# Kernel tuning notes

Measured on AMD Instinct MI355X. Metric: run time of the kernel, lower is better.

Reference implementation:

```python
import jax, jax.numpy as jnp
import numpy as np

N, E = 50000, 800000
IN, EIN, HID, OUT = 128, 64, 64, 64
NEG_SLOPE = 0.2


def setup_inputs() -> dict:
    key = jax.random.key(0)
    ks = jax.random.split(key, 24)
    p = lambda k, shape: jax.random.normal(k, shape, jnp.float32) * 0.05
    return {
        'x': jax.random.normal(ks[0], (N, IN), jnp.float32),
        'edge_index': jax.random.randint(ks[1], (2, E), 0, N, jnp.int64),
        'edge_attr': jax.random.normal(ks[2], (E, EIN), jnp.float32),
        'batch': jnp.sort(jax.random.randint(ks[3], (N,), 0, 64, jnp.int64)),
        # GATConv 1 (in -> hidden, edge_dim=EIN)
        'W1': p(ks[4], (IN, HID)), 'a_src1': p(ks[5], (HID,)), 'a_dst1': p(ks[6], (HID,)),
        'We1': p(ks[7], (EIN, HID)), 'a_e1': p(ks[8], (HID,)), 'b1': jnp.zeros((HID,), jnp.float32),
        # GATConv 2 (hidden -> out)
        'W2': p(ks[9], (HID, OUT)), 'a_src2': p(ks[10], (OUT,)), 'a_dst2': p(ks[11], (OUT,)),
        'We2': p(ks[12], (EIN, OUT)), 'a_e2': p(ks[13], (OUT,)), 'b2': jnp.zeros((OUT,), jnp.float32),
        # edge MLP
        'Wm1': p(ks[14], (EIN, HID)), 'bm1': jnp.zeros((HID,), jnp.float32),
        'Wm2': p(ks[15], (HID, OUT)), 'bm2': jnp.zeros((OUT,), jnp.float32),
    }


def _gat(x, src, dst, edge_attr, W, a_s, a_d, We, a_e, b, n):
    # PyG GATConv (heads=1): add self-loops with edge_attr fill_value='mean'
    ones = jnp.ones((src.shape[0],), x.dtype)
    deg = jax.ops.segment_sum(ones, dst, num_segments=n)
    loop_attr = jax.ops.segment_sum(edge_attr, dst, num_segments=n) / jnp.maximum(deg, 1.0)[:, None]
    ar = jnp.arange(n)
    src2 = jnp.concatenate([src, ar])
    dst2 = jnp.concatenate([dst, ar])
    ea = jnp.concatenate([edge_attr, loop_attr], axis=0)  # [E+N, EIN]
    h = x @ W                                             # [N, C]
    a_src = h @ a_s                                       # [N]
    a_dst = h @ a_d                                       # [N]
    a_edge = (ea @ We) @ a_e                              # [E+N]
    alpha = jax.nn.leaky_relu(a_src[src2] + a_dst[dst2] + a_edge, NEG_SLOPE)
    # scatter-softmax over incoming edges of each dst node
    amax = jax.ops.segment_max(alpha, dst2, num_segments=n)
    ex = jnp.exp(alpha - amax[dst2])
    denom = jax.ops.segment_sum(ex, dst2, num_segments=n)
    coef = ex / denom[dst2]                               # [E+N]
    out = jax.ops.segment_sum(h[src2] * coef[:, None], dst2, num_segments=n)
    return out + b


def reference(x, edge_index, edge_attr, batch,
              W1, a_src1, a_dst1, We1, a_e1, b1,
              W2, a_src2, a_dst2, We2, a_e2, b2,
              Wm1, bm1, Wm2, bm2):
    n = x.shape[0]
    src, dst = edge_index[0], edge_index[1]
    h = _gat(x, src, dst, edge_attr, W1, a_src1, a_dst1, We1, a_e1, b1, n)
    h = jax.nn.elu(h)
    h = _gat(h, src, dst, edge_attr, W2, a_src2, a_dst2, We2, a_e2, b2, n)
    e = jax.nn.relu(edge_attr @ Wm1 + bm1) @ Wm2 + bm2
    return h, e, batch
```

## Files before the change

### kernel.cpp

```cpp
#include <hip/hip_runtime.h>

constexpr int NN = 50000;
constexpr int NE = 800000;
constexpr int C = 64;
constexpr int IN_DIM = 128;
constexpr float NEG = 0.2f;
constexpr int NB = (NN + 255) / 256;

typedef __attribute__((ext_vector_type(8))) short short8;
typedef __attribute__((ext_vector_type(4))) float f32x4;

__device__ __forceinline__ unsigned short f2bf(float f) {
    unsigned u = __float_as_uint(f);
    unsigned r = 0x7FFFu + ((u >> 16) & 1u);
    return (unsigned short)((u + r) >> 16);
}
__device__ __forceinline__ unsigned pack_bf2(float a, float b) {
    return (unsigned)f2bf(a) | ((unsigned)f2bf(b) << 16);
}
__device__ __forceinline__ float bf2f(unsigned u) {
    return __uint_as_float(u << 16);
}

__global__ __launch_bounds__(256) void k_setup(
        const float* __restrict__ We1, const float* __restrict__ ae1v,
        const float* __restrict__ We2, const float* __restrict__ ae2v,
        const float* __restrict__ W1, const float* __restrict__ as1,
        const float* __restrict__ ad1,
        const float* __restrict__ W2, const float* __restrict__ as2,
        const float* __restrict__ ad2,
        const int* __restrict__ batch,
        float* __restrict__ vecs, int* __restrict__ hist, int* __restrict__ bagg,
        float* __restrict__ out_b) {
    int t = blockIdx.x * 256 + threadIdx.x;
    if (t < 512) {
        const float* M; const float* v; int row;
        if      (t < 64)  { M = We1; v = ae1v; row = t; }
        else if (t < 128) { M = We2; v = ae2v; row = t - 64; }
        else if (t < 256) { M = W1;  v = as1;  row = t - 128; }
        else if (t < 384) { M = W1;  v = ad1;  row = t - 256; }
        else if (t < 448) { M = W2;  v = as2;  row = t - 384; }
        else              { M = W2;  v = ad2;  row = t - 448; }
        float s = 0.f;
        #pragma unroll
        for (int c = 0; c < 64; ++c) s += M[row * 64 + c] * v[c];
        vecs[t] = s;
    }
    if (t < NN) { hist[t] = 0; out_b[t] = (float)batch[t]; }
    if (t < NB) bagg[t] = 0;
}

__global__ __launch_bounds__(256) void k_mlp_mfma(
        const float* __restrict__ ea, const int* __restrict__ dst,
        const float* __restrict__ Wm1, const float* __restrict__ bm1,
        const float* __restrict__ Wm2, const float* __restrict__ bm2,
        const float* __restrict__ wv,
        float* __restrict__ eout, float* __restrict__ ae1, float* __restrict__ ae2,
        int* __restrict__ hist) {
    constexpr int AP = 144;
    __shared__ char Atile[128 * AP];
    __shared__ char Bt1[64 * AP];
    __shared__ char Bt2[64 * AP];
    const int t = threadIdx.x;
    const long long E0 = (long long)blockIdx.x * 128;
    const int l = t & 63;

    if (t < 128) atomicAdd(&hist[dst[E0 + t]], 1);

    {
        const int j = t & 15;
        const int eb = t >> 4;
        float4 wk1 = *(const float4*)&wv[j * 4];
        float4 wk2 = *(const float4*)&wv[64 + j * 4];
        const f32x4* g = (const f32x4*)(ea + E0 * 64);
        float s1[8], s2[8];
        #pragma unroll
        for (int q = 0; q < 8; ++q) {
            f32x4 v = __builtin_nontemporal_load(&g[t + 256 * q]);
            int e = eb + 16 * q;
            s1[q] = v[0] * wk1.x + v[1] * wk1.y + v[2] * wk1.z + v[3] * wk1.w;
            s2[q] = v[0] * wk2.x + v[1] * wk2.y + v[2] * wk2.z + v[3] * wk2.w;
            uint2 wr;
            wr.x = pack_bf2(v[0], v[1]);
            wr.y = pack_bf2(v[2], v[3]);
            *(uint2*)(Atile + e * AP + j * 8) = wr;
        }
        #pragma unroll
        for (int off = 1; off < 16; off <<= 1) {
            #pragma unroll
            for (int q = 0; q < 8; ++q) {
                s1[q] += __shfl_xor(s1[q], off);
                s2[q] += __shfl_xor(s2[q], off);
            }
        }
        float o1 = 0.f, o2 = 0.f;
        #pragma unroll
        for (int q = 0; q < 8; ++q) {
            if (j == q)     o1 = s1[q];
            if (j == q + 8) o2 = s2[q];
        }
        if (j < 8) ae1[E0 + eb + 16 * j] = o1;
        else       ae2[E0 + eb + 16 * (j - 8)] = o2;
    }
    {
        const int c = t & 63, kq = t >> 6;
        #pragma unroll
        for (int i = 0; i < 16; i += 2) {
            int k = kq * 16 + i;
            *(unsigned*)(Bt1 + c * AP + k * 2) = pack_bf2(Wm1[k * 64 + c], Wm1[(k + 1) * 64 + c]);
            *(unsigned*)(Bt2 + c * AP + k * 2) = pack_bf2(Wm2[k * 64 + c], Wm2[(k + 1) * 64 + c]);
        }
    }
    __syncthreads();

    const int m0 = (t >> 6) * 32;
    const int lr = l & 15;
    const int lq = l >> 4;
    const int lk = lq * 8;

    f32x4 acc[4][2] = {};
    #pragma unroll
    for (int ks = 0; ks < 2; ++ks) {
        int ko = ks * 32 + lk;
        short8 a0 = *(const short8*)(Atile + (m0 + lr) * AP + ko * 2);
        short8 a1 = *(const short8*)(Atile + (m0 + 16 + lr) * AP + ko * 2);
        #pragma unroll
        for (int ct = 0; ct < 4; ++ct) {
            short8 b = *(const short8*)(Bt1 + (ct * 16 + lr) * AP + ko * 2);
            acc[ct][0] = __builtin_amdgcn_mfma_f32_16x16x32_bf16(b, a0, acc[ct][0], 0, 0, 0);
            acc[ct][1] = __builtin_amdgcn_mfma_f32_16x16x32_bf16(b, a1, acc[ct][1], 0, 0, 0);
        }
    }
    #pragma unroll
    for (int ct = 0; ct < 4; ++ct) {
        float4 bv = *(const float4*)&bm1[ct * 16 + lq * 4];
        #pragma unroll
        for (int et = 0; et < 2; ++et) {
            float v0 = fmaxf(acc[ct][et][0] + bv.x, 0.f);
            float v1 = fmaxf(acc[ct][et][1] + bv.y, 0.f);
            float v2 = fmaxf(acc[ct][et][2] + bv.z, 0.f);
            float v3 = fmaxf(acc[ct][et][3] + bv.w, 0.f);
            uint2 w;
            w.x = pack_bf2(v0, v1);
            w.y = pack_bf2(v2, v3);
            int e = m0 + et * 16 + lr;
            *(uint2*)(Atile + e * AP + (ct * 16 + lq * 4) * 2) = w;
        }
    }
    f32x4 acc2[4][2] = {};
    #pragma unroll
    for (int ks = 0; ks < 2; ++ks) {
        int ko = ks * 32 + lk;
        short8 a0 = *(const short8*)(Atile + (m0 + lr) * AP + ko * 2);
        short8 a1 = *(const short8*)(Atile + (m0 + 16 + lr) * AP + ko * 2);
        #pragma unroll
        for (int ct = 0; ct < 4; ++ct) {
            short8 b = *(const short8*)(Bt2 + (ct * 16 + lr) * AP + ko * 2);
            acc2[ct][0] = __builtin_amdgcn_mfma_f32_16x16x32_bf16(b, a0, acc2[ct][0], 0, 0, 0);
            acc2[ct][1] = __builtin_amdgcn_mfma_f32_16x16x32_bf16(b, a1, acc2[ct][1], 0, 0, 0);
        }
    }
    #pragma unroll
    for (int ct = 0; ct < 4; ++ct) {
        float4 bv = *(const float4*)&bm2[ct * 16 + lq * 4];
        #pragma unroll
        for (int et = 0; et < 2; ++et) {
            int e = m0 + et * 16 + lr;
            f32x4 o;
            o[0] = acc2[ct][et][0] + bv.x;
            o[1] = acc2[ct][et][1] + bv.y;
            o[2] = acc2[ct][et][2] + bv.z;
            o[3] = acc2[ct][et][3] + bv.w;
            __builtin_nontemporal_store(o, (f32x4*)&eout[(E0 + e) * 64 + ct * 16 + lq * 4]);
        }
    }
}

template <int K, bool BF16IN>
__global__ __launch_bounds__(256) void k_feat_mfma(
        const void* __restrict__ xv, const float* __restrict__ W,
        const float* __restrict__ uv,
        unsigned short* __restrict__ h, float* __restrict__ asrc,
        float* __restrict__ adst, int M) {
    constexpr int AP = K * 2 + 16;
    constexpr int QW = K / 4;
    constexpr int NQ = K / 8;
    constexpr int EPQ = 256 / QW;
    __shared__ char Atile[128 * AP];
    __shared__ char Bt[64 * AP];
    const int t = threadIdx.x;
    const int M0 = blockIdx.x * 128;
    const int l = t & 63;

    {
        const int j = t % QW;
        const int eb = t / QW;
        float4 wk1 = *(const float4*)&uv[j * 4];
        float4 wk2 = *(const float4*)&uv[K + j * 4];
        float s1[NQ], s2[NQ];
        #pragma unroll
        for (int q = 0; q < NQ; ++q) {
            int e = eb + EPQ * q;
            float v0, v1, v2, v3;
            uint2 wr;
            if constexpr (BF16IN) {
                const uint2* g = (const uint2*)xv + (long long)M0 * (K / 4);
                uint2 w = make_uint2(0u, 0u);
                if (M0 + e < M) w = g[t + 256 * q];
                v0 = bf2f(w.x & 0xFFFFu); v1 = bf2f(w.x >> 16);
                v2 = bf2f(w.y & 0xFFFFu); v3 = bf2f(w.y >> 16);
                wr = w;
            } else {
                const float4* g = (const float4*)xv + (long long)M0 * (K / 4);
                float4 v = make_float4(0.f, 0.f, 0.f, 0.f);
                if (M0 + e < M) v = g[t + 256 * q];
                v0 = v.x; v1 = v.y; v2 = v.z; v3 = v.w;
                wr.x = pack_bf2(v.x, v.y);
                wr.y = pack_bf2(v.z, v.w);
            }
            s1[q] = v0 * wk1.x + v1 * wk1.y + v2 * wk1.z + v3 * wk1.w;
            s2[q] = v0 * wk2.x + v1 * wk2.y + v2 * wk2.z + v3 * wk2.w;
            *(uint2*)(Atile + e * AP + j * 8) = wr;
        }
        #pragma unroll
        for (int off = 1; off < QW; off <<= 1) {
            #pragma unroll
            for (int q = 0; q < NQ; ++q) {
                s1[q] += __shfl_xor(s1[q], off);
                s2[q] += __shfl_xor(s2[q], off);
            }
        }
        float o1 = 0.f, o2 = 0.f;
        #pragma unroll
        for (int q = 0; q < NQ; ++q) {
            if (j == q)      o1 = s1[q];
            if (j == q + NQ) o2 = s2[q];
        }
        if (j < NQ) { int e = eb + EPQ * j;        if (M0 + e < M) asrc[M0 + e] = o1; }
        else        { int e = eb + EPQ * (j - NQ); if (M0 + e < M) adst[M0 + e] = o2; }
    }
    {
        const int c = t & 63, kq = t >> 6;
        #pragma unroll
        for (int i = 0; i < K / 4; i += 2) {
            int k = kq * (K / 4) + i;
            *(unsigned*)(Bt + c * AP + k * 2) = pack_bf2(W[k * 64 + c], W[(k + 1) * 64 + c]);
        }
    }
    __syncthreads();

    const int m0 = (t >> 6) * 32;
    const int lr = l & 15;
    const int lq = l >> 4;
    const int lk = lq * 8;

    f32x4 acc[4][2] = {};
    #pragma unroll
    for (int ks = 0; ks < K / 32; ++ks) {
        int ko = ks * 32 + lk;
        short8 a0 = *(const short8*)(Atile + (m0 + lr) * AP + ko * 2);
        short8 a1 = *(const short8*)(Atile + (m0 + 16 + lr) * AP + ko * 2);
        #pragma unroll
        for (int ct = 0; ct < 4; ++ct) {
            short8 b = *(const short8*)(Bt + (ct * 16 + lr) * AP + ko * 2);
            acc[ct][0] = __builtin_amdgcn_mfma_f32_16x16x32_bf16(b, a0, acc[ct][0], 0, 0, 0);
            acc[ct][1] = __builtin_amdgcn_mfma_f32_16x16x32_bf16(b, a1, acc[ct][1], 0, 0, 0);
        }
    }
    #pragma unroll
    for (int ct = 0; ct < 4; ++ct)
    #pragma unroll
    for (int et = 0; et < 2; ++et) {
        int row = m0 + et * 16 + lr;
        if (M0 + row < M) {
            uint2 w;
            w.x = pack_bf2(acc[ct][et][0], acc[ct][et][1]);
            w.y = pack_bf2(acc[ct][et][2], acc[ct][et][3]);
            *(uint2*)&h[(long long)(M0 + row) * 64 + ct * 16 + lq * 4] = w;
        }
    }
}

__global__ __launch_bounds__(256) void k_scan_f(const int* __restrict__ hist,
        int* __restrict__ row_ptr, int* __restrict__ cursor, int* __restrict__ bagg) {
    __shared__ int s[256];
    __shared__ int red[5];
    const int t = threadIdx.x, b = blockIdx.x;
    const int idx = b * 256 + t;
    int v = (idx < NN) ? hist[idx] : 0;
    s[t] = v;
    __syncthreads();
    #pragma unroll
    for (int off = 1; off < 256; off <<= 1) {
        int x = (t >= off) ? s[t - off] : 0;
        __syncthreads();
        s[t] += x;
        __syncthreads();
    }
    if (t == 255)
        __hip_atomic_store(&bagg[b], (s[255] << 1) | 1,
                           __ATOMIC_RELEASE, __HIP_MEMORY_SCOPE_AGENT);
    int contrib = 0;
    if (t < b) {
        int a;
        do {
            a = __hip_atomic_load(&bagg[t], __ATOMIC_ACQUIRE, __HIP_MEMORY_SCOPE_AGENT);
        } while (!(a & 1));
        contrib = a >> 1;
    }
    #pragma unroll
    for (int off = 32; off; off >>= 1) contrib += __shfl_down(contrib, off);
    if ((t & 63) == 0) red[t >> 6] = contrib;
    __syncthreads();
    if (t == 0) red[4] = red[0] + red[1] + red[2] + red[3];
    __syncthreads();
    int offset = red[4];
    if (idx < NN) {
        int rp = offset + s[t] - v;
        row_ptr[idx] = rp;
        cursor[idx] = rp;
    }
    if (idx == NN) row_ptr[NN] = NE;
}

__global__ void k_scatter(const int* __restrict__ src, const int* __restrict__ dst,
                          const float* __restrict__ ae1, const float* __restrict__ ae2,
                          int* __restrict__ cursor, uint2* __restrict__ csr) {
    int t = blockIdx.x * blockDim.x + threadIdx.x;
    if (t >= NE) return;
    int d = dst[t];
    int pos = atomicAdd(&cursor[d], 1);
    csr[pos] = make_uint2((unsigned)src[t], pack_bf2(ae1[t], ae2[t]));
}

template <bool IS_L1>
__global__ void k_gat(const int* __restrict__ row_ptr, const uint2* __restrict__ csr,
                      const float* __restrict__ asrc, const float* __restrict__ adst,
                      const unsigned short* __restrict__ h, const float* __restrict__ bias,
                      void* __restrict__ outv) {
    int n = blockIdx.x * 4 + (threadIdx.x >> 6);
    if (n >= NN) return;
    int lane = threadIdx.x & 63;
    int g = lane >> 4, s = lane & 15;
    int beg = row_ptr[n], end = row_ptr[n + 1];
    float adn = adst[n];
    float m = -1e30f, l = 0.f, sum_ae = 0.f;
    float4 acc = make_float4(0.f, 0.f, 0.f, 0.f);

    int i = beg + g;
    uint2 rc = make_uint2(0u, 0u);
    ushort4 hu = make_ushort4(0, 0, 0, 0);
    float asv = 0.f;
    if (i < end) {
        rc = csr[i];
        hu = *(const ushort4*)&h[(long long)rc.x * 64 + s * 4];
        asv = asrc[rc.x];
    }
    for (; i < end; i += 4) {
        uint2 rn = rc; ushort4 hn = hu; float asn = asv;
        if (i + 4 < end) {
            rn = csr[i + 4];
            hn = *(const ushort4*)&h[(long long)rn.x * 64 + s * 4];
            asn = asrc[rn.x];
        }
        float ae = IS_L1 ? bf2f(rc.y & 0xFFFFu) : bf2f(rc.y >> 16);
        sum_ae += ae;
        float a = asv + adn + ae;
        a = a > 0.f ? a : NEG * a;
        float mn = fmaxf(m, a);
        float sc = __expf(m - mn), p = __expf(a - mn);
        l = l * sc + p;
        acc.x = acc.x * sc + p * bf2f(hu.x);
        acc.y = acc.y * sc + p * bf2f(hu.y);
        acc.z = acc.z * sc + p * bf2f(hu.z);
        acc.w = acc.w * sc + p * bf2f(hu.w);
        m = mn;
        rc = rn; hu = hn; asv = asn;
    }
    #pragma unroll
    for (int off = 16; off < 64; off <<= 1) {
        float mo = __shfl_xor(m, off);
        float lo = __shfl_xor(l, off);
        float ax = __shfl_xor(acc.x, off);
        float ay = __shfl_xor(acc.y, off);
        float az = __shfl_xor(acc.z, off);
        float aw = __shfl_xor(acc.w, off);
        float so = __shfl_xor(sum_ae, off);
        float mn = fmaxf(m, mo);
        float s1 = __expf(m - mn), s2 = __expf(mo - mn);
        l = l * s1 + lo * s2;
        acc.x = acc.x * s1 + ax * s2;
        acc.y = acc.y * s1 + ay * s2;
        acc.z = acc.z * s1 + az * s2;
        acc.w = acc.w * s1 + aw * s2;
        sum_ae += so;
        m = mn;
    }
    {
        float deg = (float)(end - beg);
        float ae = sum_ae / fmaxf(deg, 1.f);
        float a = asrc[n] + adn + ae;
        a = a > 0.f ? a : NEG * a;
        ushort4 hun = *(const ushort4*)&h[(long long)n * 64 + s * 4];
        float mn = fmaxf(m, a);
        float sc = __expf(m - mn), p = __expf(a - mn);
        l = l * sc + p;
        acc.x = acc.x * sc + p * bf2f(hun.x);
        acc.y = acc.y * sc + p * bf2f(hun.y);
        acc.z = acc.z * sc + p * bf2f(hun.z);
        acc.w = acc.w * sc + p * bf2f(hun.w);
    }
    if (g == 0) {
        float4 o;
        o.x = acc.x / l + bias[s * 4 + 0];
        o.y = acc.y / l + bias[s * 4 + 1];
        o.z = acc.z / l + bias[s * 4 + 2];
        o.w = acc.w / l + bias[s * 4 + 3];
        if (IS_L1) {
            o.x = o.x > 0.f ? o.x : expm1f(o.x);
            o.y = o.y > 0.f ? o.y : expm1f(o.y);
            o.z = o.z > 0.f ? o.z : expm1f(o.z);
            o.w = o.w > 0.f ? o.w : expm1f(o.w);
            uint2 w;
            w.x = pack_bf2(o.x, o.y);
            w.y = pack_bf2(o.z, o.w);
            *(uint2*)&((unsigned short*)outv)[(long long)n * 64 + s * 4] = w;
        } else {
            *(float4*)&((float*)outv)[(long long)n * 64 + s * 4] = o;
        }
    }
}

extern "C" void kernel_launch(void* const* d_in, const int* in_sizes, int n_in,
                              void* d_out, int out_size, void* d_ws, size_t ws_size,
                              hipStream_t stream) {
    const float* x     = (const float*)d_in[0];
    const int*   eidx  = (const int*)d_in[1];
    const float* eattr = (const float*)d_in[2];
    const int*   batch = (const int*)d_in[3];
    const float* W1 = (const float*)d_in[4];
    const float* as1 = (const float*)d_in[5];
    const float* ad1 = (const float*)d_in[6];
    const float* We1 = (const float*)d_in[7];
    const float* vae1 = (const float*)d_in[8];
    const float* b1  = (const float*)d_in[9];
    const float* W2 = (const float*)d_in[10];
    const float* as2 = (const float*)d_in[11];
    const float* ad2 = (const float*)d_in[12];
    const float* We2 = (const float*)d_in[13];
    const float* vae2 = (const float*)d_in[14];
    const float* b2  = (const float*)d_in[15];
    const float* Wm1 = (const float*)d_in[16];
    const float* bm1 = (const float*)d_in[17];
    const float* Wm2 = (const float*)d_in[18];
    const float* bm2 = (const float*)d_in[19];

    const int* src = eidx;
    const int* dst = eidx + NE;

    float* out_h = (float*)d_out;
    float* out_e = out_h + (long long)NN * C;
    float* out_b = out_e + (long long)NE * C;

    uint2* csr    = (uint2*)d_ws;
    float* ae1    = (float*)(csr + NE);
    float* ae2    = ae1 + NE;
    unsigned short* out1b = (unsigned short*)(ae2 + NE);
    unsigned short* h = out1b + (long long)NN * C;
    float* asrc   = (float*)(h + (long long)NN * C);
    float* adst   = asrc + NN;
    float* vecs   = adst + NN;
    int*   hist   = (int*)(vecs + 512);
    int*   row_ptr= hist + NN;
    int*   cursor = row_ptr + NN + 1;
    int*   bagg   = cursor + NN;

    k_setup<<<NB, 256, 0, stream>>>(We1, vae1, We2, vae2, W1, as1, ad1,
                                    W2, as2, ad2, batch, vecs, hist, bagg, out_b);

    k_mlp_mfma<<<NE / 128, 256, 0, stream>>>(eattr, dst, Wm1, bm1, Wm2, bm2, vecs,
                                             out_e, ae1, ae2, hist);

    k_scan_f<<<NB, 256, 0, stream>>>(hist, row_ptr, cursor, bagg);
    k_scatter<<<(NE + 255) / 256, 256, 0, stream>>>(src, dst, ae1, ae2, cursor, csr);

    k_feat_mfma<IN_DIM, false><<<(NN + 127) / 128, 256, 0, stream>>>(x, W1, vecs + 128,
                                                                     h, asrc, adst, NN);
    k_gat<true><<<(NN + 3) / 4, 256, 0, stream>>>(row_ptr, csr, asrc, adst, h, b1, out1b);

    k_feat_mfma<C, true><<<(NN + 127) / 128, 256, 0, stream>>>(out1b, W2, vecs + 384,
                                                               h, asrc, adst, NN);
    k_gat<false><<<(NN + 3) / 4, 256, 0, stream>>>(row_ptr, csr, asrc, adst, h, b2, out_h);
}
```

Before: 281.2 us.

## Pre-transpose MLP weights to bf16 once and drop per-block LDS staging

Converts Wm1/Wm2 to transposed bf16 arrays once in the setup kernel and has the MFMA edge-MLP kernel read B fragments directly from global memory (L2-cached) instead of staging them into LDS in every block. Each wave now loads and stages only its own 32 edges, so the block-wide __syncthreads is removed and LDS use shrinks, which can raise occupancy. The cost is that the B fragments are now reloaded from global/L2 by every wave instead of read from LDS.

```diff
diff --git a/kernel.cpp b/kernel.cpp
--- a/kernel.cpp
+++ b/kernel.cpp
@@ -29,8 +29,11 @@
         const float* __restrict__ ad1,
         const float* __restrict__ W2, const float* __restrict__ as2,
         const float* __restrict__ ad2,
+        const float* __restrict__ Wm1, const float* __restrict__ Wm2,
         const int* __restrict__ batch,
-        float* __restrict__ vecs, int* __restrict__ hist, int* __restrict__ bagg,
+        float* __restrict__ vecs, unsigned short* __restrict__ wt1g,
+        unsigned short* __restrict__ wt2g,
+        int* __restrict__ hist, int* __restrict__ bagg,
         float* __restrict__ out_b) {
     int t = blockIdx.x * 256 + threadIdx.x;
     if (t < 512) {
@@ -46,44 +49,51 @@
         for (int c = 0; c < 64; ++c) s += M[row * 64 + c] * v[c];
         vecs[t] = s;
     }
+    if (t < 4096) {
+        int c = t >> 6, k = t & 63;
+        wt1g[t] = f2bf(Wm1[k * 64 + c]);
+    } else if (t < 8192) {
+        int u = t - 4096;
+        int c = u >> 6, k = u & 63;
+        wt2g[u] = f2bf(Wm2[k * 64 + c]);
+    }
     if (t < NN) { hist[t] = 0; out_b[t] = (float)batch[t]; }
     if (t < NB) bagg[t] = 0;
 }
 
 __global__ __launch_bounds__(256) void k_mlp_mfma(
         const float* __restrict__ ea, const int* __restrict__ dst,
-        const float* __restrict__ Wm1, const float* __restrict__ bm1,
-        const float* __restrict__ Wm2, const float* __restrict__ bm2,
+        const unsigned short* __restrict__ wt1g, const float* __restrict__ bm1,
+        const unsigned short* __restrict__ wt2g, const float* __restrict__ bm2,
         const float* __restrict__ wv,
         float* __restrict__ eout, float* __restrict__ ae1, float* __restrict__ ae2,
         int* __restrict__ hist) {
     constexpr int AP = 144;
     __shared__ char Atile[128 * AP];
-    __shared__ char Bt1[64 * AP];
-    __shared__ char Bt2[64 * AP];
     const int t = threadIdx.x;
     const long long E0 = (long long)blockIdx.x * 128;
     const int l = t & 63;
+    const int m0 = (t >> 6) * 32;
 
     if (t < 128) atomicAdd(&hist[dst[E0 + t]], 1);
 
     {
-        const int j = t & 15;
-        const int eb = t >> 4;
+        const int j = l & 15;
+        const int eb = l >> 4;
         float4 wk1 = *(const float4*)&wv[j * 4];
         float4 wk2 = *(const float4*)&wv[64 + j * 4];
-        const f32x4* g = (const f32x4*)(ea + E0 * 64);
+        const f32x4* g = (const f32x4*)(ea + (E0 + m0) * 64);
         float s1[8], s2[8];
         #pragma unroll
         for (int q = 0; q < 8; ++q) {
-            f32x4 v = __builtin_nontemporal_load(&g[t + 256 * q]);
-            int e = eb + 16 * q;
+            int e = eb + 4 * q;
+            f32x4 v = __builtin_nontemporal_load(&g[e * 16 + j]);
             s1[q] = v[0] * wk1.x + v[1] * wk1.y + v[2] * wk1.z + v[3] * wk1.w;
             s2[q] = v[0] * wk2.x + v[1] * wk2.y + v[2] * wk2.z + v[3] * wk2.w;
             uint2 wr;
             wr.x = pack_bf2(v[0], v[1]);
             wr.y = pack_bf2(v[2], v[3]);
-            *(uint2*)(Atile + e * AP + j * 8) = wr;
+            *(uint2*)(Atile + (m0 + e) * AP + j * 8) = wr;
         }
         #pragma unroll
         for (int off = 1; off < 16; off <<= 1) {
@@ -99,21 +109,10 @@
             if (j == q)     o1 = s1[q];
             if (j == q + 8) o2 = s2[q];
         }
-        if (j < 8) ae1[E0 + eb + 16 * j] = o1;
-        else       ae2[E0 + eb + 16 * (j - 8)] = o2;
-    }
-    {
-        const int c = t & 63, kq = t >> 6;
-        #pragma unroll
-        for (int i = 0; i < 16; i += 2) {
-            int k = kq * 16 + i;
-            *(unsigned*)(Bt1 + c * AP + k * 2) = pack_bf2(Wm1[k * 64 + c], Wm1[(k + 1) * 64 + c]);
-            *(unsigned*)(Bt2 + c * AP + k * 2) = pack_bf2(Wm2[k * 64 + c], Wm2[(k + 1) * 64 + c]);
-        }
-    }
-    __syncthreads();
-
-    const int m0 = (t >> 6) * 32;
+        if (j < 8) ae1[E0 + m0 + eb + 4 * j] = o1;
+        else       ae2[E0 + m0 + eb + 4 * (j - 8)] = o2;
+    }
+
     const int lr = l & 15;
     const int lq = l >> 4;
     const int lk = lq * 8;
@@ -126,7 +125,7 @@
         short8 a1 = *(const short8*)(Atile + (m0 + 16 + lr) * AP + ko * 2);
         #pragma unroll
         for (int ct = 0; ct < 4; ++ct) {
-            short8 b = *(const short8*)(Bt1 + (ct * 16 + lr) * AP + ko * 2);
+            short8 b = *(const short8*)&wt1g[(ct * 16 + lr) * 64 + ko];
             acc[ct][0] = __builtin_amdgcn_mfma_f32_16x16x32_bf16(b, a0, acc[ct][0], 0, 0, 0);
             acc[ct][1] = __builtin_amdgcn_mfma_f32_16x16x32_bf16(b, a1, acc[ct][1], 0, 0, 0);
         }
@@ -155,7 +154,7 @@
         short8 a1 = *(const short8*)(Atile + (m0 + 16 + lr) * AP + ko * 2);
         #pragma unroll
         for (int ct = 0; ct < 4; ++ct) {
-            short8 b = *(const short8*)(Bt2 + (ct * 16 + lr) * AP + ko * 2);
+            short8 b = *(const short8*)&wt2g[(ct * 16 + lr) * 64 + ko];
             acc2[ct][0] = __builtin_amdgcn_mfma_f32_16x16x32_bf16(b, a0, acc2[ct][0], 0, 0, 0);
             acc2[ct][1] = __builtin_amdgcn_mfma_f32_16x16x32_bf16(b, a1, acc2[ct][1], 0, 0, 0);
         }
@@ -470,15 +469,18 @@
     float* asrc   = (float*)(h + (long long)NN * C);
     float* adst   = asrc + NN;
     float* vecs   = adst + NN;
-    int*   hist   = (int*)(vecs + 512);
+    unsigned short* wt1g = (unsigned short*)(vecs + 512);
+    unsigned short* wt2g = wt1g + 4096;
+    int*   hist   = (int*)(wt2g + 4096);
     int*   row_ptr= hist + NN;
     int*   cursor = row_ptr + NN + 1;
     int*   bagg   = cursor + NN;
 
     k_setup<<<NB, 256, 0, stream>>>(We1, vae1, We2, vae2, W1, as1, ad1,
-                                    W2, as2, ad2, batch, vecs, hist, bagg, out_b);
-
-    k_mlp_mfma<<<NE / 128, 256, 0, stream>>>(eattr, dst, Wm1, bm1, Wm2, bm2, vecs,
+                                    W2, as2, ad2, Wm1, Wm2, batch,
+                                    vecs, wt1g, wt2g, hist, bagg, out_b);
+
+    k_mlp_mfma<<<NE / 128, 256, 0, stream>>>(eattr, dst, wt1g, bm1, wt2g, bm2, vecs,
                                              out_e, ae1, ae2, hist);
 
     k_scan_f<<<NB, 256, 0, stream>>>(hist, row_ptr, cursor, bagg);
```

Measured after the change: 305.3 us. +8.6%, slower.
